# Performance work log

Measured on AMD Instinct MI355X. Metric: run time of the kernel, lower is better.

Reference implementation:

```python
import jax, jax.numpy as jnp
import numpy as np

N_NODES = 20000
N_EDGES = 320000
D_IN = 256
DIMS = [512, 256, 128]
NEG_SLOPE = 0.2


def gatv2(x, src, dst, Wl, Wr, att, b, n):
    # GATv2Conv (heads=1, no self loops, no edge_attr)
    xl = x @ Wl                      # [N, D] source transform (lin_l)
    xr = x @ Wr                      # [N, D] target transform (lin_r)
    e = jax.nn.leaky_relu(xl[src] + xr[dst], NEG_SLOPE) @ att  # [E]
    # segment softmax over destination nodes
    m = jax.ops.segment_max(e, dst, num_segments=n)
    ex = jnp.exp(e - m[dst])
    s = jax.ops.segment_sum(ex, dst, num_segments=n)
    alpha = ex / (s[dst] + 1e-16)
    out = jax.ops.segment_sum(alpha[:, None] * xl[src], dst, num_segments=n)
    return out + b


def setup_inputs() -> dict:
    key = jax.random.key(0)
    ks = jax.random.split(key, 32)
    x = jax.random.normal(ks[0], (N_NODES, D_IN), dtype=jnp.float32)
    edge_index = jax.random.randint(ks[1], (2, N_EDGES), 0, N_NODES, dtype=jnp.int32)
    inp = {"x": x, "edge_index": edge_index}
    d_in = D_IN
    ki = 2
    for li, d_out in enumerate(DIMS, start=1):
        sc = 1.0 / np.sqrt(d_in)
        inp[f"Wl{li}"] = jax.random.normal(ks[ki + 0], (d_in, d_out), dtype=jnp.float32) * sc
        inp[f"Wr{li}"] = jax.random.normal(ks[ki + 1], (d_in, d_out), dtype=jnp.float32) * sc
        inp[f"att{li}"] = jax.random.normal(ks[ki + 2], (d_out,), dtype=jnp.float32) * (1.0 / np.sqrt(d_out))
        inp[f"bc{li}"] = jnp.zeros((d_out,), dtype=jnp.float32)
        inp[f"Ws{li}"] = jax.random.normal(ks[ki + 3], (d_in, d_out), dtype=jnp.float32) * sc
        inp[f"bs{li}"] = jnp.zeros((d_out,), dtype=jnp.float32)
        ki += 4
        d_in = d_out
    return inp


def reference(x, edge_index,
              Wl1, Wr1, att1, bc1, Ws1, bs1,
              Wl2, Wr2, att2, bc2, Ws2, bs2,
              Wl3, Wr3, att3, bc3, Ws3, bs3):
    src, dst = edge_index[0], edge_index[1]
    n = x.shape[0]
    h = gatv2(x, src, dst, Wl1, Wr1, att1, bc1, n) + (x @ Ws1 + bs1)
    h = jax.nn.relu(h)
    h = gatv2(h, src, dst, Wl2, Wr2, att2, bc2, n) + (h @ Ws2 + bs2)
    h = jax.nn.relu(h)
    h = gatv2(h, src, dst, Wl3, Wr3, att3, bc3, n) + (h @ Ws3 + bs3)
    return h
```

## Files before the change

### kernel.cpp

```cpp
#include <hip/hip_runtime.h>
#include <hip/hip_bf16.h>
#include <math.h>

#define N_NODES 20000
#define N_EDGES 320000

typedef _Float16 f16x8 __attribute__((ext_vector_type(8)));
typedef _Float16 h2 __attribute__((ext_vector_type(2)));
typedef float f32x4 __attribute__((ext_vector_type(4)));

__device__ __forceinline__ unsigned short f2h_bits(float f) {
    _Float16 h = (_Float16)f;
    return __builtin_bit_cast(unsigned short, h);
}

typedef const unsigned int __attribute__((address_space(1)))* gas_ptr;
typedef unsigned int __attribute__((address_space(3)))* las_ptr;
__device__ __forceinline__ void gld16(const unsigned short* g, unsigned short* l) {
    __builtin_amdgcn_global_load_lds((gas_ptr)(const void*)g, (las_ptr)(void*)l, 16, 0, 0);
}

__global__ void zero_int_kernel(int* __restrict__ p, int n) {
    int i = blockIdx.x * blockDim.x + threadIdx.x;
    if (i < n) p[i] = 0;
}

__global__ void count_deg_kernel(const int* __restrict__ dst, int* __restrict__ deg, int E) {
    int i = blockIdx.x * blockDim.x + threadIdx.x;
    if (i < E) atomicAdd(&deg[dst[i]], 1);
}

#define SCAN_T 1024
#define SCAN_C 20
__global__ __launch_bounds__(1024) void scan_kernel(const int* __restrict__ deg,
                                                    int* __restrict__ offs,
                                                    int* __restrict__ cursor, int n) {
    __shared__ int sd[SCAN_T];
    int t = threadIdx.x;
    int base = t * SCAN_C;
    int vex[SCAN_C];
    int run = 0;
#pragma unroll
    for (int k = 0; k < SCAN_C; ++k) {
        int i = base + k;
        int d = (i < n) ? deg[i] : 0;
        vex[k] = run;
        run += d;
    }
    sd[t] = run;
    __syncthreads();
    for (int off = 1; off < SCAN_T; off <<= 1) {
        int x = (t >= off) ? sd[t - off] : 0;
        __syncthreads();
        sd[t] += x;
        __syncthreads();
    }
    int excl = sd[t] - run;
#pragma unroll
    for (int k = 0; k < SCAN_C; ++k) {
        int i = base + k;
        if (i < n) { int e = excl + vex[k]; offs[i] = e; cursor[i] = e; }
    }
    if (t == SCAN_T - 1) offs[n] = sd[t];
}

__global__ void scatter_kernel(const int* __restrict__ src, const int* __restrict__ dst,
                               int* __restrict__ cursor, int* __restrict__ csr_src, int E) {
    int i = blockIdx.x * blockDim.x + threadIdx.x;
    if (i < E) {
        int pos = atomicAdd(&cursor[dst[i]], 1);
        csr_src[pos] = src[i];
    }
}

struct PrepJobs {
    const float* W[9];
    unsigned short* Wt[9];
    int K[9];
    int D[9];
    int beg[10];
    const float* x;
    unsigned short* xh;
    int nconv4;
};
__global__ void prep_kernel(PrepJobs jb) {
    int i = blockIdx.x * blockDim.x + threadIdx.x;
    int nt = jb.beg[9];
    if (i < nt) {
        int job = 0;
        while (i >= jb.beg[job + 1]) ++job;
        int local = i - jb.beg[job];
        int D = jb.D[job], K = jb.K[job];
        int d = local / K, k = local - d * K;
        jb.Wt[job][local] = f2h_bits(jb.W[job][(size_t)k * D + d]);
    } else {
        int c = i - nt;
        if (c < jb.nconv4) {
            int base = c * 4;
            float4 v = *(const float4*)(jb.x + base);
            uint2 pk;
            pk.x = (unsigned int)f2h_bits(v.x) | ((unsigned int)f2h_bits(v.y) << 16);
            pk.y = (unsigned int)f2h_bits(v.z) | ((unsigned int)f2h_bits(v.w) << 16);
            *(uint2*)(jb.xh + base) = pk;
        }
    }
}

template <int SEED_F32>
__global__ __launch_bounds__(256) void gemm3_kernel(
        const unsigned short* __restrict__ A,
        const unsigned short* __restrict__ Bt,
        unsigned short* __restrict__ xlh,
        unsigned short* __restrict__ xrh,
        unsigned short* __restrict__ seedh,
        float* __restrict__ seedf,
        const float* __restrict__ b1,
        const float* __restrict__ b2,
        int M, int K, int D) {
    __shared__ __align__(16) unsigned short Asl[128 * 32];
    __shared__ __align__(16) unsigned short Bsl[128 * 32];

    int NC = (3 * D) >> 7;
    int MT = (M + 127) >> 7;
    int g = blockIdx.x;
    int xcd = g & 7, slot = g >> 3;
    int m_local = slot / NC, c = slot - m_local * NC;
    int mt = m_local * 8 + xcd;
    if (mt >= MT) return;

    int tid = threadIdx.x;
    int wave = tid >> 6, lane = tid & 63;
    int q = lane >> 4, t = lane & 15;
    int wm = (wave & 1) * 64, wn = (wave >> 1) * 64;
    int bm = mt << 7;
    int bn_all = c << 7;
    int seg = bn_all / D;
    int bn = bn_all - seg * D;

    f32x4 acc[4][4];
#pragma unroll
    for (int i = 0; i < 4; ++i)
#pragma unroll
        for (int j = 0; j < 4; ++j) acc[i][j] = (f32x4){0.f, 0.f, 0.f, 0.f};

    for (int k0 = 0; k0 < K; k0 += 32) {
#pragma unroll
        for (int rnd = 0; rnd < 2; ++rnd) {
            int ch = rnd * 256 + tid;
            int row = ch >> 2, part = ch & 3;
            int gr = bm + row; if (gr >= M) gr = M - 1;
            gld16(A + (size_t)gr * K + k0 + part * 8,
                  Asl + (rnd * 256 + wave * 64) * 8);
        }
#pragma unroll
        for (int rnd = 0; rnd < 2; ++rnd) {
            int ch = rnd * 256 + tid;
            int row = ch >> 2, part = ch & 3;
            gld16(Bt + (size_t)(bn_all + row) * K + k0 + part * 8,
                  Bsl + (rnd * 256 + wave * 64) * 8);
        }
        __syncthreads();

        f16x8 an[4], am[4];
#pragma unroll
        for (int jn = 0; jn < 4; ++jn)
            an[jn] = *(const f16x8*)(Bsl + (wn + jn * 16 + t) * 32 + q * 8);
#pragma unroll
        for (int im = 0; im < 4; ++im)
            am[im] = *(const f16x8*)(Asl + (wm + im * 16 + t) * 32 + q * 8);
#pragma unroll
        for (int jn = 0; jn < 4; ++jn)
#pragma unroll
            for (int im = 0; im < 4; ++im)
                acc[jn][im] = __builtin_amdgcn_mfma_f32_16x16x32_f16(an[jn], am[im], acc[jn][im], 0, 0, 0);
        __syncthreads();
    }

#pragma unroll
    for (int jn = 0; jn < 4; ++jn) {
        int n0 = bn + wn + jn * 16 + q * 4;
        float bx = 0.f, by = 0.f, bz = 0.f, bw = 0.f;
        if (seg == 2) {
            float4 bb1 = *(const float4*)(b1 + n0);
            float4 bb2 = *(const float4*)(b2 + n0);
            bx = bb1.x + bb2.x; by = bb1.y + bb2.y;
            bz = bb1.z + bb2.z; bw = bb1.w + bb2.w;
        }
#pragma unroll
        for (int im = 0; im < 4; ++im) {
            int m = bm + wm + im * 16 + t;
            if (m < M) {
                float v0 = acc[jn][im][0] + bx;
                float v1 = acc[jn][im][1] + by;
                float v2 = acc[jn][im][2] + bz;
                float v3 = acc[jn][im][3] + bw;
                size_t idx = (size_t)m * D + n0;
                if (seg == 2 && SEED_F32) {
                    *(float4*)(seedf + idx) = make_float4(v0, v1, v2, v3);
                } else {
                    uint2 pk;
                    pk.x = (unsigned int)f2h_bits(v0) | ((unsigned int)f2h_bits(v1) << 16);
                    pk.y = (unsigned int)f2h_bits(v2) | ((unsigned int)f2h_bits(v3) << 16);
                    unsigned short* dstp = (seg == 0) ? xlh : (seg == 1) ? xrh : seedh;
                    *(uint2*)(dstp + idx) = pk;
                }
            }
        }
    }
}

template <int D, int SEED_H, int WRITE_H, int RELU>
__global__ __launch_bounds__(128) void fused_agg_kernel(
        const unsigned short* __restrict__ xl,
        const unsigned short* __restrict__ xr,
        const float* __restrict__ att,
        const int* __restrict__ offs,
        const int* __restrict__ csr_src,
        const unsigned short* __restrict__ seedh,
        const float* __restrict__ seedf,
        float* __restrict__ outf,
        unsigned short* __restrict__ outh) {
    constexpr int VPL = D / 64;
    constexpr int HP = VPL / 2;
    typedef _Float16 hvec __attribute__((ext_vector_type(VPL)));

    int wave = threadIdx.x >> 6, lane = threadIdx.x & 63;
    int n = blockIdx.x * 2 + wave;
    if (n >= N_NODES) return;
    int beg = offs[n], end = offs[n + 1];

    h2 xr_h[HP], att_h[HP];
    hvec xrv = *(const hvec*)(xr + (size_t)n * D + lane * VPL);
#pragma unroll
    for (int pp = 0; pp < HP; ++pp) {
        xr_h[pp] = (h2){xrv[2 * pp], xrv[2 * pp + 1]};
        att_h[pp] = (h2){(_Float16)att[lane * VPL + 2 * pp],
                         (_Float16)att[lane * VPL + 2 * pp + 1]};
    }

    float acc[VPL];
#pragma unroll
    for (int v = 0; v < VPL; ++v) acc[v] = 0.f;
    float m = -INFINITY, s = 0.f;

    const _Float16 c02 = (_Float16)0.2f;
    int lb0 = lane & 1;
    int lb1 = lane & 2;

    int nfull = (end - beg) >> 2;
    int j = beg;
    int i0 = 0, i1 = 0, i2 = 0, i3 = 0;
    if (nfull > 0) {
        i0 = csr_src[beg]; i1 = csr_src[beg + 1];
        i2 = csr_src[beg + 2]; i3 = csr_src[beg + 3];
    }
    for (int b = 0; b < nfull; ++b) {
        int s0 = i0, s1 = i1, s2 = i2, s3 = i3;
        int jn4 = j + 4;
        if (b + 1 < nfull) {
            i0 = csr_src[jn4]; i1 = csr_src[jn4 + 1];
            i2 = csr_src[jn4 + 2]; i3 = csr_src[jn4 + 3];
        }
        hvec x0 = *(const hvec*)(xl + (size_t)s0 * D + lane * VPL);
        hvec x1 = *(const hvec*)(xl + (size_t)s1 * D + lane * VPL);
        hvec x2 = *(const hvec*)(xl + (size_t)s2 * D + lane * VPL);
        hvec x3 = *(const hvec*)(xl + (size_t)s3 * D + lane * VPL);
        float p0 = 0.f, p1 = 0.f, p2 = 0.f, p3 = 0.f;
#pragma unroll
        for (int pp = 0; pp < HP; ++pp) {
            h2 a0 = (h2){x0[2 * pp], x0[2 * pp + 1]};
            h2 a1 = (h2){x1[2 * pp], x1[2 * pp + 1]};
            h2 a2 = (h2){x2[2 * pp], x2[2 * pp + 1]};
            h2 a3 = (h2){x3[2 * pp], x3[2 * pp + 1]};
            h2 z0 = a0 + xr_h[pp];
            h2 z1 = a1 + xr_h[pp];
            h2 z2 = a2 + xr_h[pp];
            h2 z3 = a3 + xr_h[pp];
            h2 l0 = __builtin_elementwise_max(z0, z0 * c02);
            h2 l1 = __builtin_elementwise_max(z1, z1 * c02);
            h2 l2 = __builtin_elementwise_max(z2, z2 * c02);
            h2 l3 = __builtin_elementwise_max(z3, z3 * c02);
#if __has_builtin(__builtin_amdgcn_fdot2)
            p0 = __builtin_amdgcn_fdot2(l0, att_h[pp], p0, false);
            p1 = __builtin_amdgcn_fdot2(l1, att_h[pp], p1, false);
            p2 = __builtin_amdgcn_fdot2(l2, att_h[pp], p2, false);
            p3 = __builtin_amdgcn_fdot2(l3, att_h[pp], p3, false);
#else
            p0 += (float)l0.x * (float)att_h[pp].x + (float)l0.y * (float)att_h[pp].y;
            p1 += (float)l1.x * (float)att_h[pp].x + (float)l1.y * (float)att_h[pp].y;
            p2 += (float)l2.x * (float)att_h[pp].x + (float)l2.y * (float)att_h[pp].y;
            p3 += (float)l3.x * (float)att_h[pp].x + (float)l3.y * (float)att_h[pp].y;
#endif
        }
        float k0 = lb0 ? p1 : p0, sn0 = lb0 ? p0 : p1;
        float k1 = lb0 ? p3 : p2, sn1 = lb0 ? p2 : p3;
        k0 += __shfl_xor(sn0, 1, 64);
        k1 += __shfl_xor(sn1, 1, 64);
        float k = lb1 ? k1 : k0, sn = lb1 ? k0 : k1;
        k += __shfl_xor(sn, 2, 64);
        k += __shfl_xor(k, 4, 64);
        k += __shfl_xor(k, 8, 64);
        k += __shfl_xor(k, 16, 64);
        k += __shfl_xor(k, 32, 64);
        float q0 = __shfl(k, 0, 64);
        float q1 = __shfl(k, 1, 64);
        float q2 = __shfl(k, 2, 64);
        float q3 = __shfl(k, 3, 64);

        float mn = fmaxf(m, fmaxf(fmaxf(q0, q1), fmaxf(q2, q3)));
        float sc = __expf(m - mn);
        float e0 = __expf(q0 - mn);
        float e1 = __expf(q1 - mn);
        float e2 = __expf(q2 - mn);
        float e3 = __expf(q3 - mn);
        s = s * sc + e0 + e1 + e2 + e3;
#pragma unroll
        for (int v = 0; v < VPL; ++v)
            acc[v] = acc[v] * sc + e0 * (float)x0[v] + e1 * (float)x1[v]
                                 + e2 * (float)x2[v] + e3 * (float)x3[v];
        m = mn;
        j = jn4;
    }
    for (; j < end; ++j) {
        int s0 = csr_src[j];
        hvec x0 = *(const hvec*)(xl + (size_t)s0 * D + lane * VPL);
        float p0 = 0.f;
#pragma unroll
        for (int pp = 0; pp < HP; ++pp) {
            h2 a0 = (h2){x0[2 * pp], x0[2 * pp + 1]};
            h2 z0 = a0 + xr_h[pp];
            h2 l0 = __builtin_elementwise_max(z0, z0 * c02);
#if __has_builtin(__builtin_amdgcn_fdot2)
            p0 = __builtin_amdgcn_fdot2(l0, att_h[pp], p0, false);
#else
            p0 += (float)l0.x * (float)att_h[pp].x + (float)l0.y * (float)att_h[pp].y;
#endif
        }
#pragma unroll
        for (int o = 32; o > 0; o >>= 1) p0 += __shfl_xor(p0, o, 64);
        float mn = fmaxf(m, p0);
        float sc = __expf(m - mn);
        float e0 = __expf(p0 - mn);
        s = s * sc + e0;
#pragma unroll
        for (int v = 0; v < VPL; ++v) acc[v] = acc[v] * sc + e0 * (float)x0[v];
        m = mn;
    }

    float sinv = 1.0f / (s + 1e-16f);
    size_t base = (size_t)n * D + lane * VPL;
    float sd[VPL];
    if (SEED_H) {
        hvec sv = *(const hvec*)(seedh + base);
#pragma unroll
        for (int v = 0; v < VPL; ++v) sd[v] = (float)sv[v];
    } else {
#pragma unroll
        for (int v = 0; v < VPL; ++v) sd[v] = seedf[base + v];
    }
#pragma unroll
    for (int v = 0; v < VPL; ++v) {
        float val = sd[v] + acc[v] * sinv;
        if (RELU) val = fmaxf(val, 0.f);
        if (WRITE_H) outh[base + v] = f2h_bits(val);
        else         outf[base + v] = val;
    }
}

static void run_layer(const unsigned short* hact, int K, int D,
                      const unsigned short* Wcat,
                      const float* att, const float* bc, const float* bs,
                      unsigned short* xlh, unsigned short* xrh,
                      unsigned short* seedh, float* seedf,
                      const int* offs, const int* csr_src,
                      float* outf, unsigned short* outh, int final_layer,
                      hipStream_t stream) {
    int NC = 3 * D / 128;
    int MT = (N_NODES + 127) / 128;
    int nblk = 8 * ((MT + 7) / 8) * NC;
    if (final_layer)
        hipLaunchKernelGGL((gemm3_kernel<1>), dim3(nblk), dim3(256), 0, stream, hact, Wcat,
                           xlh, xrh, (unsigned short*)nullptr, seedf, bs, bc, N_NODES, K, D);
    else
        hipLaunchKernelGGL((gemm3_kernel<0>), dim3(nblk), dim3(256), 0, stream, hact, Wcat,
                           xlh, xrh, seedh, (float*)nullptr, bs, bc, N_NODES, K, D);

    dim3 agrid((N_NODES + 1) / 2);
    if (D == 512) {
        hipLaunchKernelGGL((fused_agg_kernel<512, 1, 1, 1>), agrid, dim3(128), 0, stream,
                           xlh, xrh, att, offs, csr_src, seedh, (const float*)nullptr,
                           (float*)nullptr, outh);
    } else if (D == 256) {
        hipLaunchKernelGGL((fused_agg_kernel<256, 1, 1, 1>), agrid, dim3(128), 0, stream,
                           xlh, xrh, att, offs, csr_src, seedh, (const float*)nullptr,
                           (float*)nullptr, outh);
    } else {
        hipLaunchKernelGGL((fused_agg_kernel<128, 0, 0, 0>), agrid, dim3(128), 0, stream,
                           xlh, xrh, att, offs, csr_src, (const unsigned short*)nullptr, seedf,
                           outf, (unsigned short*)nullptr);
    }
}

extern "C" void kernel_launch(void* const* d_in, const int* in_sizes, int n_in,
                              void* d_out, int out_size, void* d_ws, size_t ws_size,
                              hipStream_t stream) {
    const float* x = (const float*)d_in[0];
    const int* ei = (const int*)d_in[1];
    const int* src = ei;
    const int* dst = ei + N_EDGES;

    const float* Wl1 = (const float*)d_in[2];
    const float* Wr1 = (const float*)d_in[3];
    const float* att1 = (const float*)d_in[4];
    const float* bc1 = (const float*)d_in[5];
    const float* Ws1 = (const float*)d_in[6];
    const float* bs1 = (const float*)d_in[7];
    const float* Wl2 = (const float*)d_in[8];
    const float* Wr2 = (const float*)d_in[9];
    const float* att2 = (const float*)d_in[10];
    const float* bc2 = (const float*)d_in[11];
    const float* Ws2 = (const float*)d_in[12];
    const float* bs2 = (const float*)d_in[13];
    const float* Wl3 = (const float*)d_in[14];
    const float* Wr3 = (const float*)d_in[15];
    const float* att3 = (const float*)d_in[16];
    const float* bc3 = (const float*)d_in[17];
    const float* Ws3 = (const float*)d_in[18];
    const float* bs3 = (const float*)d_in[19];

    const size_t NF = (size_t)N_NODES * 512;
    const size_t NH = (size_t)N_NODES * 256;
    unsigned short* xlh   = (unsigned short*)d_ws;
    unsigned short* xrh   = xlh + NF;
    unsigned short* seedh = xrh + NF;
    unsigned short* xhf   = seedh + NF;
    unsigned short* h1h   = xhf + NH;
    unsigned short* h2h   = h1h + NF;
    unsigned short* Wcat1 = h2h + NH;
    unsigned short* Wcat2 = Wcat1 + 3 * 512 * 256;
    unsigned short* Wcat3 = Wcat2 + 3 * 256 * 512;
    int* deg     = (int*)(Wcat3 + 3 * 128 * 256);
    int* offs    = deg + N_NODES;
    int* cursor  = offs + N_NODES + 1;
    int* csr_src = cursor + N_NODES;
    size_t needed = (size_t)((char*)(csr_src + N_EDGES) - (char*)d_ws);
    if (ws_size < needed) return;

    hipLaunchKernelGGL(zero_int_kernel, dim3((N_NODES + 255) / 256), dim3(256), 0, stream,
                       deg, N_NODES);
    hipLaunchKernelGGL(count_deg_kernel, dim3((N_EDGES + 255) / 256), dim3(256), 0, stream,
                       dst, deg, N_EDGES);
    hipLaunchKernelGGL(scan_kernel, dim3(1), dim3(SCAN_T), 0, stream, deg, offs, cursor, N_NODES);
    hipLaunchKernelGGL(scatter_kernel, dim3((N_EDGES + 255) / 256), dim3(256), 0, stream,
                       src, dst, cursor, csr_src, N_EDGES);

    {
        PrepJobs jb;
        const float* Ws_[9]  = {Wl1, Wr1, Ws1, Wl2, Wr2, Ws2, Wl3, Wr3, Ws3};
        unsigned short* Wt_[9] = {Wcat1, Wcat1 + 512 * 256, Wcat1 + 2 * 512 * 256,
                                  Wcat2, Wcat2 + 256 * 512, Wcat2 + 2 * 256 * 512,
                                  Wcat3, Wcat3 + 128 * 256, Wcat3 + 2 * 128 * 256};
        int K_[9] = {256, 256, 256, 512, 512, 512, 256, 256, 256};
        int D_[9] = {512, 512, 512, 256, 256, 256, 128, 128, 128};
        int o = 0;
        for (int i = 0; i < 9; ++i) {
            jb.W[i] = Ws_[i]; jb.Wt[i] = Wt_[i]; jb.K[i] = K_[i]; jb.D[i] = D_[i];
            jb.beg[i] = o; o += K_[i] * D_[i];
        }
        jb.beg[9] = o;
        jb.x = x;
        jb.xh = xhf;
        jb.nconv4 = N_NODES * 256 / 4;
        int total = o + jb.nconv4;
        hipLaunchKernelGGL(prep_kernel, dim3((total + 255) / 256), dim3(256), 0, stream, jb);
    }

    run_layer(xhf, 256, 512, Wcat1, att1, bc1, bs1,
              xlh, xrh, seedh, (float*)nullptr, offs, csr_src,
              (float*)nullptr, h1h, 0, stream);
    run_layer(h1h, 512, 256, Wcat2, att2, bc2, bs2,
              xlh, xrh, seedh, (float*)nullptr, offs, csr_src,
              (float*)nullptr, h2h, 0, stream);
    run_layer(h2h, 256, 128, Wcat3, att3, bc3, bs3,
              xlh, xrh, (unsigned short*)nullptr, (float*)d_out, offs, csr_src,
              (float*)d_out, (unsigned short*)nullptr, 1, stream);
}
```

Measured before the change: 367.1 us.

## Double-buffer neighbor feature gathers into LDS via async global_load_lds

Replaces direct register gathers of source-node feature rows in the fused aggregation loop with asynchronous global-to-LDS DMA into a per-wave double buffer. The next batch of four rows is prefetched while the current one is computed, and edge indices are loaded one batch further ahead and broadcast by lane shuffles. The goal is to hide gather latency behind the attention/softmax math. It adds LDS traffic and fixed vmcnt waits that depend on the exact count of outstanding loads, which is fragile if the compiler reorders or adds memory ops.

Measured after the change: 367.8 us. Within noise of the previous version (+0.2%).

```diff
diff --git a/kernel.cpp b/kernel.cpp
--- a/kernel.cpp
+++ b/kernel.cpp
@@ -209,6 +209,35 @@
     }
 }
 
+template <int D>
+__device__ __forceinline__ void dma_batch(const unsigned short* __restrict__ xl,
+                                          int i0, int i1, int i2, int i3,
+                                          unsigned short* dst, int lane) {
+    if constexpr (D == 512) {
+        gld16(xl + (size_t)i0 * D + lane * 8, dst);
+        gld16(xl + (size_t)i1 * D + lane * 8, dst + D);
+        gld16(xl + (size_t)i2 * D + lane * 8, dst + 2 * D);
+        gld16(xl + (size_t)i3 * D + lane * 8, dst + 3 * D);
+    } else if constexpr (D == 256) {
+        int ra = (lane & 32) ? i1 : i0;
+        int rb = (lane & 32) ? i3 : i2;
+        gld16(xl + (size_t)ra * D + (lane & 31) * 8, dst);
+        gld16(xl + (size_t)rb * D + (lane & 31) * 8, dst + 2 * D);
+    } else {
+        int a = (lane & 16) ? i1 : i0;
+        int b = (lane & 16) ? i3 : i2;
+        int r = (lane & 32) ? b : a;
+        gld16(xl + (size_t)r * D + (lane & 15) * 8, dst);
+    }
+}
+
+template <int D>
+__device__ __forceinline__ void wait_dma() {
+    if constexpr (D == 512)      asm volatile("s_waitcnt vmcnt(5)" ::: "memory");
+    else if constexpr (D == 256) asm volatile("s_waitcnt vmcnt(3)" ::: "memory");
+    else                         asm volatile("s_waitcnt vmcnt(2)" ::: "memory");
+}
+
 template <int D, int SEED_H, int WRITE_H, int RELU>
 __global__ __launch_bounds__(128) void fused_agg_kernel(
         const unsigned short* __restrict__ xl,
@@ -224,6 +253,8 @@
     constexpr int HP = VPL / 2;
     typedef _Float16 hvec __attribute__((ext_vector_type(VPL)));
 
+    __shared__ __align__(16) unsigned short lbuf[2][2][4 * D];
+
     int wave = threadIdx.x >> 6, lane = threadIdx.x & 63;
     int n = blockIdx.x * 2 + wave;
     if (n >= N_NODES) return;
@@ -249,77 +280,89 @@
 
     int nfull = (end - beg) >> 2;
     int j = beg;
-    int i0 = 0, i1 = 0, i2 = 0, i3 = 0;
+    unsigned short* lw = &lbuf[wave][0][0];
+
     if (nfull > 0) {
-        i0 = csr_src[beg]; i1 = csr_src[beg + 1];
-        i2 = csr_src[beg + 2]; i3 = csr_src[beg + 3];
-    }
-    for (int b = 0; b < nfull; ++b) {
-        int s0 = i0, s1 = i1, s2 = i2, s3 = i3;
-        int jn4 = j + 4;
-        if (b + 1 < nfull) {
-            i0 = csr_src[jn4]; i1 = csr_src[jn4 + 1];
-            i2 = csr_src[jn4 + 2]; i3 = csr_src[jn4 + 3];
-        }
-        hvec x0 = *(const hvec*)(xl + (size_t)s0 * D + lane * VPL);
-        hvec x1 = *(const hvec*)(xl + (size_t)s1 * D + lane * VPL);
-        hvec x2 = *(const hvec*)(xl + (size_t)s2 * D + lane * VPL);
-        hvec x3 = *(const hvec*)(xl + (size_t)s3 * D + lane * VPL);
-        float p0 = 0.f, p1 = 0.f, p2 = 0.f, p3 = 0.f;
-#pragma unroll
-        for (int pp = 0; pp < HP; ++pp) {
-            h2 a0 = (h2){x0[2 * pp], x0[2 * pp + 1]};
-            h2 a1 = (h2){x1[2 * pp], x1[2 * pp + 1]};
-            h2 a2 = (h2){x2[2 * pp], x2[2 * pp + 1]};
-            h2 a3 = (h2){x3[2 * pp], x3[2 * pp + 1]};
-            h2 z0 = a0 + xr_h[pp];
-            h2 z1 = a1 + xr_h[pp];
-            h2 z2 = a2 + xr_h[pp];
-            h2 z3 = a3 + xr_h[pp];
-            h2 l0 = __builtin_elementwise_max(z0, z0 * c02);
-            h2 l1 = __builtin_elementwise_max(z1, z1 * c02);
-            h2 l2 = __builtin_elementwise_max(z2, z2 * c02);
-            h2 l3 = __builtin_elementwise_max(z3, z3 * c02);
+        int iv0 = csr_src[beg + (lane & 3)];
+        int jn = (nfull > 1) ? beg + 4 : beg;
+        int ivc = csr_src[jn + (lane & 3)];
+        {
+            int e0 = __shfl(iv0, 0, 64), e1 = __shfl(iv0, 1, 64);
+            int e2 = __shfl(iv0, 2, 64), e3 = __shfl(iv0, 3, 64);
+            dma_batch<D>(xl, e0, e1, e2, e3, lw, lane);
+        }
+        for (int b = 0; b < nfull; ++b) {
+            int j2 = j + 8;
+            if (j2 > end - 4) j2 = end - 4;
+            int ivn = csr_src[j2 + (lane & 3)];
+            {
+                int e0 = __shfl(ivc, 0, 64), e1 = __shfl(ivc, 1, 64);
+                int e2 = __shfl(ivc, 2, 64), e3 = __shfl(ivc, 3, 64);
+                dma_batch<D>(xl, e0, e1, e2, e3, lw + ((b + 1) & 1) * 4 * D, lane);
+            }
+            wait_dma<D>();
+            const unsigned short* rb = lw + (b & 1) * (4 * D);
+            hvec x0 = *(const hvec*)(rb + 0 * D + lane * VPL);
+            hvec x1 = *(const hvec*)(rb + 1 * D + lane * VPL);
+            hvec x2 = *(const hvec*)(rb + 2 * D + lane * VPL);
+            hvec x3 = *(const hvec*)(rb + 3 * D + lane * VPL);
+            float p0 = 0.f, p1 = 0.f, p2 = 0.f, p3 = 0.f;
+#pragma unroll
+            for (int pp = 0; pp < HP; ++pp) {
+                h2 a0 = (h2){x0[2 * pp], x0[2 * pp + 1]};
+                h2 a1 = (h2){x1[2 * pp], x1[2 * pp + 1]};
+                h2 a2 = (h2){x2[2 * pp], x2[2 * pp + 1]};
+                h2 a3 = (h2){x3[2 * pp], x3[2 * pp + 1]};
+                h2 z0 = a0 + xr_h[pp];
+                h2 z1 = a1 + xr_h[pp];
+                h2 z2 = a2 + xr_h[pp];
+                h2 z3 = a3 + xr_h[pp];
+                h2 l0 = __builtin_elementwise_max(z0, z0 * c02);
+                h2 l1 = __builtin_elementwise_max(z1, z1 * c02);
+                h2 l2 = __builtin_elementwise_max(z2, z2 * c02);
+                h2 l3 = __builtin_elementwise_max(z3, z3 * c02);
 #if __has_builtin(__builtin_amdgcn_fdot2)
-            p0 = __builtin_amdgcn_fdot2(l0, att_h[pp], p0, false);
-            p1 = __builtin_amdgcn_fdot2(l1, att_h[pp], p1, false);
-            p2 = __builtin_amdgcn_fdot2(l2, att_h[pp], p2, false);
-            p3 = __builtin_amdgcn_fdot2(l3, att_h[pp], p3, false);
+                p0 = __builtin_amdgcn_fdot2(l0, att_h[pp], p0, false);
+                p1 = __builtin_amdgcn_fdot2(l1, att_h[pp], p1, false);
+                p2 = __builtin_amdgcn_fdot2(l2, att_h[pp], p2, false);
+                p3 = __builtin_amdgcn_fdot2(l3, att_h[pp], p3, false);
 #else
-            p0 += (float)l0.x * (float)att_h[pp].x + (float)l0.y * (float)att_h[pp].y;
-            p1 += (float)l1.x * (float)att_h[pp].x + (float)l1.y * (float)att_h[pp].y;
-            p2 += (float)l2.x * (float)att_h[pp].x + (float)l2.y * (float)att_h[pp].y;
-            p3 += (float)l3.x * (float)att_h[pp].x + (float)l3.y * (float)att_h[pp].y;
+                p0 += (float)l0.x * (float)att_h[pp].x + (float)l0.y * (float)att_h[pp].y;
+                p1 += (float)l1.x * (float)att_h[pp].x + (float)l1.y * (float)att_h[pp].y;
+                p2 += (float)l2.x * (float)att_h[pp].x + (float)l2.y * (float)att_h[pp].y;
+                p3 += (float)l3.x * (float)att_h[pp].x + (float)l3.y * (float)att_h[pp].y;
 #endif
-        }
-        float k0 = lb0 ? p1 : p0, sn0 = lb0 ? p0 : p1;
-        float k1 = lb0 ? p3 : p2, sn1 = lb0 ? p2 : p3;
-        k0 += __shfl_xor(sn0, 1, 64);
-        k1 += __shfl_xor(sn1, 1, 64);
-        float k = lb1 ? k1 : k0, sn = lb1 ? k0 : k1;
-        k += __shfl_xor(sn, 2, 64);
-        k += __shfl_xor(k, 4, 64);
-        k += __shfl_xor(k, 8, 64);
-        k += __shfl_xor(k, 16, 64);
-        k += __shfl_xor(k, 32, 64);
-        float q0 = __shfl(k, 0, 64);
-        float q1 = __shfl(k, 1, 64);
-        float q2 = __shfl(k, 2, 64);
-        float q3 = __shfl(k, 3, 64);
-
-        float mn = fmaxf(m, fmaxf(fmaxf(q0, q1), fmaxf(q2, q3)));
-        float sc = __expf(m - mn);
-        float e0 = __expf(q0 - mn);
-        float e1 = __expf(q1 - mn);
-        float e2 = __expf(q2 - mn);
-        float e3 = __expf(q3 - mn);
-        s = s * sc + e0 + e1 + e2 + e3;
-#pragma unroll
-        for (int v = 0; v < VPL; ++v)
-            acc[v] = acc[v] * sc + e0 * (float)x0[v] + e1 * (float)x1[v]
-                                 + e2 * (float)x2[v] + e3 * (float)x3[v];
-        m = mn;
-        j = jn4;
+            }
+            float k0 = lb0 ? p1 : p0, sn0 = lb0 ? p0 : p1;
+            float k1 = lb0 ? p3 : p2, sn1 = lb0 ? p2 : p3;
+            k0 += __shfl_xor(sn0, 1, 64);
+            k1 += __shfl_xor(sn1, 1, 64);
+            float k = lb1 ? k1 : k0, sn = lb1 ? k0 : k1;
+            k += __shfl_xor(sn, 2, 64);
+            k += __shfl_xor(k, 4, 64);
+            k += __shfl_xor(k, 8, 64);
+            k += __shfl_xor(k, 16, 64);
+            k += __shfl_xor(k, 32, 64);
+            float q0 = __shfl(k, 0, 64);
+            float q1 = __shfl(k, 1, 64);
+            float q2 = __shfl(k, 2, 64);
+            float q3 = __shfl(k, 3, 64);
+
+            float mn = fmaxf(m, fmaxf(fmaxf(q0, q1), fmaxf(q2, q3)));
+            float sc = __expf(m - mn);
+            float e0 = __expf(q0 - mn);
+            float e1 = __expf(q1 - mn);
+            float e2 = __expf(q2 - mn);
+            float e3 = __expf(q3 - mn);
+            s = s * sc + e0 + e1 + e2 + e3;
+#pragma unroll
+            for (int v = 0; v < VPL; ++v)
+                acc[v] = acc[v] * sc + e0 * (float)x0[v] + e1 * (float)x1[v]
+                                     + e2 * (float)x2[v] + e3 * (float)x3[v];
+            m = mn;
+            ivc = ivn;
+            j += 4;
+        }
     }
     for (; j < end; ++j) {
         int s0 = csr_src[j];
```

## Tile weight transpose through shared memory and double GEMM K-step to 64

Applied to the files above, without the earlier changes.

The weight prep kernel now transposes in 32x32 tiles staged through shared memory, so both the reads and the writes are coalesced. Before, each thread did a strided gather. Separately, the GEMM now loads a K-slice of 64 per iteration instead of 32 and runs two MFMA sub-steps per barrier pair. This halves the number of sync and load rounds and enlarges the load batches. The cost is double the LDS per block, which may lower occupancy, and the unpadded LDS layout may raise bank conflicts.

Measured after the change: 364.2 us. No clear change (-0.8%).

```diff
diff --git a/kernel.cpp b/kernel.cpp
--- a/kernel.cpp
+++ b/kernel.cpp
@@ -78,25 +78,40 @@
     unsigned short* Wt[9];
     int K[9];
     int D[9];
-    int beg[10];
+    int tbeg[10];
     const float* x;
     unsigned short* xh;
     int nconv4;
 };
-__global__ void prep_kernel(PrepJobs jb) {
-    int i = blockIdx.x * blockDim.x + threadIdx.x;
-    int nt = jb.beg[9];
-    if (i < nt) {
+__global__ __launch_bounds__(256) void prep_kernel(PrepJobs jb) {
+    int bid = blockIdx.x;
+    int ntile = jb.tbeg[9];
+    if (bid < ntile) {
+        __shared__ float ld[32][33];
         int job = 0;
-        while (i >= jb.beg[job + 1]) ++job;
-        int local = i - jb.beg[job];
-        int D = jb.D[job], K = jb.K[job];
-        int d = local / K, k = local - d * K;
-        jb.Wt[job][local] = f2h_bits(jb.W[job][(size_t)k * D + d]);
+        while (bid >= jb.tbeg[job + 1]) ++job;
+        int tl = bid - jb.tbeg[job];
+        int K = jb.K[job], D = jb.D[job];
+        int TK = K >> 5;
+        int td = tl / TK, tk = tl - td * TK;
+        int k0 = tk << 5, d0 = td << 5;
+        int t = threadIdx.x;
+        int c = t & 31, r0 = (t >> 5) << 2;
+        const float* Wp = jb.W[job];
+#pragma unroll
+        for (int jj = 0; jj < 4; ++jj)
+            ld[r0 + jj][c] = Wp[(size_t)(k0 + r0 + jj) * D + d0 + c];
+        __syncthreads();
+        unsigned short* Wtp = jb.Wt[job];
+#pragma unroll
+        for (int jj = 0; jj < 4; ++jj) {
+            int dr = r0 + jj;
+            Wtp[(size_t)(d0 + dr) * K + k0 + c] = f2h_bits(ld[c][dr]);
+        }
     } else {
-        int c = i - nt;
-        if (c < jb.nconv4) {
-            int base = c * 4;
+        int cidx = (bid - ntile) * 256 + (int)threadIdx.x;
+        if (cidx < jb.nconv4) {
+            int base = cidx * 4;
             float4 v = *(const float4*)(jb.x + base);
             uint2 pk;
             pk.x = (unsigned int)f2h_bits(v.x) | ((unsigned int)f2h_bits(v.y) << 16);
@@ -117,8 +132,8 @@
         const float* __restrict__ b1,
         const float* __restrict__ b2,
         int M, int K, int D) {
-    __shared__ __align__(16) unsigned short Asl[128 * 32];
-    __shared__ __align__(16) unsigned short Bsl[128 * 32];
+    __shared__ __align__(16) unsigned short Asl[128 * 64];
+    __shared__ __align__(16) unsigned short Bsl[128 * 64];
 
     int NC = (3 * D) >> 7;
     int MT = (M + 127) >> 7;
@@ -143,36 +158,39 @@
 #pragma unroll
         for (int j = 0; j < 4; ++j) acc[i][j] = (f32x4){0.f, 0.f, 0.f, 0.f};
 
-    for (int k0 = 0; k0 < K; k0 += 32) {
-#pragma unroll
-        for (int rnd = 0; rnd < 2; ++rnd) {
+    for (int k0 = 0; k0 < K; k0 += 64) {
+#pragma unroll
+        for (int rnd = 0; rnd < 4; ++rnd) {
             int ch = rnd * 256 + tid;
-            int row = ch >> 2, part = ch & 3;
+            int row = ch >> 3, part = ch & 7;
             int gr = bm + row; if (gr >= M) gr = M - 1;
             gld16(A + (size_t)gr * K + k0 + part * 8,
                   Asl + (rnd * 256 + wave * 64) * 8);
         }
 #pragma unroll
-        for (int rnd = 0; rnd < 2; ++rnd) {
+        for (int rnd = 0; rnd < 4; ++rnd) {
             int ch = rnd * 256 + tid;
-            int row = ch >> 2, part = ch & 3;
+            int row = ch >> 3, part = ch & 7;
             gld16(Bt + (size_t)(bn_all + row) * K + k0 + part * 8,
                   Bsl + (rnd * 256 + wave * 64) * 8);
         }
         __syncthreads();
 
-        f16x8 an[4], am[4];
-#pragma unroll
-        for (int jn = 0; jn < 4; ++jn)
-            an[jn] = *(const f16x8*)(Bsl + (wn + jn * 16 + t) * 32 + q * 8);
-#pragma unroll
-        for (int im = 0; im < 4; ++im)
-            am[im] = *(const f16x8*)(Asl + (wm + im * 16 + t) * 32 + q * 8);
-#pragma unroll
-        for (int jn = 0; jn < 4; ++jn)
+#pragma unroll
+        for (int kk = 0; kk < 2; ++kk) {
+            f16x8 an[4], am[4];
+#pragma unroll
+            for (int jn = 0; jn < 4; ++jn)
+                an[jn] = *(const f16x8*)(Bsl + (wn + jn * 16 + t) * 64 + kk * 32 + q * 8);
 #pragma unroll
             for (int im = 0; im < 4; ++im)
-                acc[jn][im] = __builtin_amdgcn_mfma_f32_16x16x32_f16(an[jn], am[im], acc[jn][im], 0, 0, 0);
+                am[im] = *(const f16x8*)(Asl + (wm + im * 16 + t) * 64 + kk * 32 + q * 8);
+#pragma unroll
+            for (int jn = 0; jn < 4; ++jn)
+#pragma unroll
+                for (int im = 0; im < 4; ++im)
+                    acc[jn][im] = __builtin_amdgcn_mfma_f32_16x16x32_f16(an[jn], am[im], acc[jn][im], 0, 0, 0);
+        }
         __syncthreads();
     }
 
@@ -465,14 +483,14 @@
         int o = 0;
         for (int i = 0; i < 9; ++i) {
             jb.W[i] = Ws_[i]; jb.Wt[i] = Wt_[i]; jb.K[i] = K_[i]; jb.D[i] = D_[i];
-            jb.beg[i] = o; o += K_[i] * D_[i];
-        }
-        jb.beg[9] = o;
+            jb.tbeg[i] = o; o += (K_[i] >> 5) * (D_[i] >> 5);
+        }
+        jb.tbeg[9] = o;
         jb.x = x;
         jb.xh = xhf;
         jb.nconv4 = N_NODES * 256 / 4;
-        int total = o + jb.nconv4;
-        hipLaunchKernelGGL(prep_kernel, dim3((total + 255) / 256), dim3(256), 0, stream, jb);
+        int nconv_blocks = (jb.nconv4 + 255) / 256;
+        hipLaunchKernelGGL(prep_kernel, dim3(o + nconv_blocks), dim3(256), 0, stream, jb);
     }
 
     run_layer(xhf, 256, 512, Wcat1, att1, bc1, bs1,
```
